# Kernel optimization log

Measured on AMD Instinct MI355X. Metric: run time of the kernel, lower is better.

## Reference

```python
import jax, jax.numpy as jnp
import numpy as np

B, N, C, OUT = 4, 512, 128, 128

def setup_inputs() -> dict:
    key = jax.random.key(0)
    k1, k2, k3 = jax.random.split(key, 3)
    adj_matrix = jax.random.bernoulli(k1, 0.1, (B, N, N)).astype(jnp.float32)
    features = jax.random.normal(k2, (B, N, C), dtype=jnp.float32)
    # xavier_uniform for Linear(2C -> OUT): weight stored here as [2C, OUT]
    limit = float(np.sqrt(6.0 / (2 * C + OUT)))
    W = jax.random.uniform(k3, (2 * C, OUT), minval=-limit, maxval=limit, dtype=jnp.float32)
    b = jnp.zeros((OUT,), dtype=jnp.float32)
    return {"adj_matrix": adj_matrix, "features": features, "W": W, "b": b}

def reference(adj_matrix, features, W, b):
    # pooling aggregator: masked max over neighbors (materializes [B,N,N,C], as in source)
    neg_inf = jnp.finfo(features.dtype).min
    mask = (adj_matrix > 0)[..., None]                      # [B,N,N,1]
    feat_nb = jnp.where(mask, features[:, None, :, :], neg_inf)  # [B,N,N,C]
    agg = jnp.max(feat_nb, axis=2)                          # [B,N,C]
    agg = jnp.where(jnp.isfinite(agg), agg, 0.0)
    neigh = jax.nn.relu(agg)
    combined = jnp.concatenate([features, neigh], axis=-1)  # [B,N,2C]
    return jnp.einsum('bnc,co->bno', combined, W) + b       # [B,N,OUT]
```

## Files before the change

kernel.cpp:

```cpp
#include <hip/hip_runtime.h>
#include <hip/hip_bf16.h>
#include <float.h>


#define Bsz 4
#define Nn  512
#define Cc  128
#define OUTn 128
#define NNODES (Bsz * Nn)
#define KK (2 * Cc)
#define ROWP 264

typedef __bf16 bf16x8 __attribute__((ext_vector_type(8)));
typedef float  f32x4  __attribute__((ext_vector_type(4)));

static __device__ __forceinline__ unsigned short f2bf(float x) {
    __hip_bfloat16 h = __float2bfloat16(x);
    return *reinterpret_cast<unsigned short*>(&h);
}
static __device__ __forceinline__ __bf16 f2bf16(float x) {
    unsigned short u = f2bf(x);
    return *reinterpret_cast<__bf16*>(&u);
}

__global__ __launch_bounds__(1024, 8) void sage_fused(
    const float* __restrict__ adj,
    const float* __restrict__ feat,
    const float* __restrict__ W,
    const float* __restrict__ bias,
    float* __restrict__ out)
{
    const int bid = blockIdx.x;
    const int w = threadIdx.x >> 6;
    const int l = threadIdx.x & 63;

    const int slot = w & 3;
    const int q    = w >> 2;
    const int node = bid * 4 + slot;
    const int b = node >> 9;
    const int i = node & (Nn - 1);

    __shared__ unsigned short nbr[16][128];
    __shared__ float2 pm[16][64];
    __shared__ unsigned short sA[16][ROWP];
    __shared__ f32x4 accbuf[8][16];

    const float* adjrow = adj + (size_t)node * Nn;
    const float2* f2 = (const float2*)(feat + (size_t)b * Nn * Cc);

    int cnt = 0;
    {
        float2 a = *(const float2*)(adjrow + q * 128 + 2 * l);
        unsigned long long mk = __ballot(a.x > 0.0f);
        int pos = __popcll(mk & ((1ull << l) - 1ull));
        if (a.x > 0.0f) nbr[w][pos] = (unsigned short)(q * 128 + 2 * l);
        cnt = __popcll(mk);
        mk = __ballot(a.y > 0.0f);
        pos = __popcll(mk & ((1ull << l) - 1ull));
        if (a.y > 0.0f) nbr[w][cnt + pos] = (unsigned short)(q * 128 + 2 * l + 1);
        cnt += __popcll(mk);
    }
    if (cnt > 0) {
        unsigned short p0 = nbr[w][0];
        int padded = (cnt + 7) & ~7;
        if (l < padded - cnt) nbr[w][cnt + l] = p0;
        cnt = padded;
    }

    float m0 = -FLT_MAX, m1 = -FLT_MAX;
    const uint4* nv = (const uint4*)&nbr[w][0];
    for (int k = 0; k < cnt; k += 8) {
        uint4 p = nv[k >> 3];
        int j0 = p.x & 0xffff, j1 = p.x >> 16;
        int j2 = p.y & 0xffff, j3 = p.y >> 16;
        int j4 = p.z & 0xffff, j5 = p.z >> 16;
        int j6 = p.w & 0xffff, j7 = p.w >> 16;
        float2 v0 = f2[j0 * 64 + l];
        float2 v1 = f2[j1 * 64 + l];
        float2 v2 = f2[j2 * 64 + l];
        float2 v3 = f2[j3 * 64 + l];
        float2 v4 = f2[j4 * 64 + l];
        float2 v5 = f2[j5 * 64 + l];
        float2 v6 = f2[j6 * 64 + l];
        float2 v7 = f2[j7 * 64 + l];
        m0 = fmaxf(m0, fmaxf(fmaxf(fmaxf(v0.x, v1.x), fmaxf(v2.x, v3.x)),
                             fmaxf(fmaxf(v4.x, v5.x), fmaxf(v6.x, v7.x))));
        m1 = fmaxf(m1, fmaxf(fmaxf(fmaxf(v0.y, v1.y), fmaxf(v2.y, v3.y)),
                             fmaxf(fmaxf(v4.y, v5.y), fmaxf(v6.y, v7.y))));
    }
    pm[w][l] = make_float2(m0, m1);
    __syncthreads();

    if (w < 4) {
        float2 a0 = pm[w][l],     a1 = pm[w + 4][l];
        float2 a2 = pm[w + 8][l], a3 = pm[w + 12][l];
        float n0 = fmaxf(fmaxf(fmaxf(a0.x, a1.x), fmaxf(a2.x, a3.x)), 0.0f);
        float n1 = fmaxf(fmaxf(fmaxf(a0.y, a1.y), fmaxf(a2.y, a3.y)), 0.0f);
        float2 s = f2[i * 64 + l];

        ushort2* crow = (ushort2*)&sA[w][0];
        ushort2 sv; sv.x = f2bf(s.x); sv.y = f2bf(s.y);
        ushort2 nn; nn.x = f2bf(n0);  nn.y = f2bf(n1);
        crow[l]      = sv;
        crow[64 + l] = nn;
    }
    __syncthreads();

    const int nt = w & 7;
    const int kh = w >> 3;
    const int frow = l & 15;
    const int koff = (l >> 4) * 8;
    const float* wp = W + nt * 16 + frow;

    f32x4 acc = {0.f, 0.f, 0.f, 0.f};
    #pragma unroll
    for (int ks = 0; ks < 4; ++ks) {
        const int kbase = kh * 128 + ks * 32 + koff;
        bf16x8 af = *(const bf16x8*)&sA[frow][kbase];
        bf16x8 bfr;
        #pragma unroll
        for (int j = 0; j < 8; ++j) {
            bfr[j] = f2bf16(wp[(size_t)(kbase + j) * OUTn]);
        }
        acc = __builtin_amdgcn_mfma_f32_16x16x32_bf16(af, bfr, acc, 0, 0, 0);
    }

    if (w >= 8 && l < 16) accbuf[nt][l] = acc;
    __syncthreads();

    if (w < 8 && l < 16) {
        f32x4 oth = accbuf[nt][l];
        const int col = l;
        const float bv = bias[nt * 16 + col];
        #pragma unroll
        for (int r = 0; r < 4; ++r) {
            out[(size_t)(bid * 4 + r) * OUTn + nt * 16 + col]
                = acc[r] + oth[r] + bv;
        }
    }
}

extern "C" void kernel_launch(void* const* d_in, const int* in_sizes, int n_in,
                              void* d_out, int out_size, void* d_ws, size_t ws_size,
                              hipStream_t stream) {
    const float* adj  = (const float*)d_in[0];
    const float* feat = (const float*)d_in[1];
    const float* W    = (const float*)d_in[2];
    const float* bias = (const float*)d_in[3];
    float* out = (float*)d_out;

    sage_fused<<<dim3(NNODES / 4), dim3(1024), 0, stream>>>(
        adj, feat, W, bias, out);
}
```

Baseline: 67.88 us.

## Pre-convert W to transposed bf16 and drop split-K reduction in fused kernel

Adds a small pre-kernel that converts W to bf16 and transposes it into the workspace, so each MFMA B-fragment becomes one contiguous 16-byte load instead of eight strided fp32 loads plus conversions. The GEMM stage now uses only 8 waves, each covering the full K, which removes the split-K accumulator exchange through shared memory and one block barrier. The self-feature row and bias are loaded early, before the aggregation phase, to hide their latency. The cost is an extra kernel launch per call, and half the waves now sit idle during the GEMM stage.

```diff
diff --git a/kernel.cpp b/kernel.cpp
--- a/kernel.cpp
+++ b/kernel.cpp
@@ -23,10 +23,22 @@
     return *reinterpret_cast<__bf16*>(&u);
 }
 
+__global__ __launch_bounds__(64) void wconv(
+    const float* __restrict__ W, __bf16* __restrict__ Wt)
+{
+    const int gid = blockIdx.x * 64 + threadIdx.x;
+    const int n  = gid >> 5;
+    const int kp = (gid & 31) * 8;
+    bf16x8 v;
+    #pragma unroll
+    for (int i = 0; i < 8; ++i) v[i] = f2bf16(W[(size_t)(kp + i) * OUTn + n]);
+    *(bf16x8*)(Wt + (size_t)n * KK + kp) = v;
+}
+
 __global__ __launch_bounds__(1024, 8) void sage_fused(
     const float* __restrict__ adj,
     const float* __restrict__ feat,
-    const float* __restrict__ W,
+    const __bf16* __restrict__ Wt,
     const float* __restrict__ bias,
     float* __restrict__ out)
 {
@@ -43,10 +55,14 @@
     __shared__ unsigned short nbr[16][128];
     __shared__ float2 pm[16][64];
     __shared__ unsigned short sA[16][ROWP];
-    __shared__ f32x4 accbuf[8][16];
 
     const float* adjrow = adj + (size_t)node * Nn;
     const float2* f2 = (const float2*)(feat + (size_t)b * Nn * Cc);
+
+    float2 selfrow = make_float2(0.f, 0.f);
+    if (w < 4) selfrow = f2[i * 64 + l];
+    float bv = 0.f;
+    if (w < 8) bv = bias[w * 16 + (l & 15)];
 
     int cnt = 0;
     {
@@ -96,46 +112,35 @@
         float2 a2 = pm[w + 8][l], a3 = pm[w + 12][l];
         float n0 = fmaxf(fmaxf(fmaxf(a0.x, a1.x), fmaxf(a2.x, a3.x)), 0.0f);
         float n1 = fmaxf(fmaxf(fmaxf(a0.y, a1.y), fmaxf(a2.y, a3.y)), 0.0f);
-        float2 s = f2[i * 64 + l];
 
         ushort2* crow = (ushort2*)&sA[w][0];
-        ushort2 sv; sv.x = f2bf(s.x); sv.y = f2bf(s.y);
-        ushort2 nn; nn.x = f2bf(n0);  nn.y = f2bf(n1);
+        ushort2 sv; sv.x = f2bf(selfrow.x); sv.y = f2bf(selfrow.y);
+        ushort2 nn; nn.x = f2bf(n0);        nn.y = f2bf(n1);
         crow[l]      = sv;
         crow[64 + l] = nn;
     }
     __syncthreads();
 
-    const int nt = w & 7;
-    const int kh = w >> 3;
-    const int frow = l & 15;
-    const int koff = (l >> 4) * 8;
-    const float* wp = W + nt * 16 + frow;
+    if (w < 8) {
+        const int nt = w;
+        const int frow = l & 15;
+        const int koff = (l >> 4) * 8;
+        const __bf16* wtp = Wt + (size_t)(nt * 16 + frow) * KK;
 
-    f32x4 acc = {0.f, 0.f, 0.f, 0.f};
-    #pragma unroll
-    for (int ks = 0; ks < 4; ++ks) {
-        const int kbase = kh * 128 + ks * 32 + koff;
-        bf16x8 af = *(const bf16x8*)&sA[frow][kbase];
-        bf16x8 bfr;
+        f32x4 acc = {0.f, 0.f, 0.f, 0.f};
         #pragma unroll
-        for (int j = 0; j < 8; ++j) {
-            bfr[j] = f2bf16(wp[(size_t)(kbase + j) * OUTn]);
+        for (int ks = 0; ks < 8; ++ks) {
+            const int kbase = ks * 32 + koff;
+            bf16x8 af  = *(const bf16x8*)&sA[frow][kbase];
+            bf16x8 bfr = *(const bf16x8*)(wtp + kbase);
+            acc = __builtin_amdgcn_mfma_f32_16x16x32_bf16(af, bfr, acc, 0, 0, 0);
         }
-        acc = __builtin_amdgcn_mfma_f32_16x16x32_bf16(af, bfr, acc, 0, 0, 0);
-    }
 
-    if (w >= 8 && l < 16) accbuf[nt][l] = acc;
-    __syncthreads();
-
-    if (w < 8 && l < 16) {
-        f32x4 oth = accbuf[nt][l];
-        const int col = l;
-        const float bv = bias[nt * 16 + col];
-        #pragma unroll
-        for (int r = 0; r < 4; ++r) {
-            out[(size_t)(bid * 4 + r) * OUTn + nt * 16 + col]
-                = acc[r] + oth[r] + bv;
+        if (l < 16) {
+            #pragma unroll
+            for (int r = 0; r < 4; ++r) {
+                out[(size_t)(bid * 4 + r) * OUTn + nt * 16 + l] = acc[r] + bv;
+            }
         }
     }
 }
@@ -148,7 +153,9 @@
     const float* W    = (const float*)d_in[2];
     const float* bias = (const float*)d_in[3];
     float* out = (float*)d_out;
+    __bf16* Wt = (__bf16*)d_ws;
 
+    wconv<<<dim3(64), dim3(64), 0, stream>>>(W, Wt);
     sage_fused<<<dim3(NNODES / 4), dim3(1024), 0, stream>>>(
-        adj, feat, W, bias, out);
+        adj, feat, Wt, bias, out);
 }
```

After: 71.13 us. 4.8% more time.
